# Kernel optimization log

Measured on AMD Instinct MI355X. Metric: run time of the kernel, lower is better.

Reference implementation:

```python
import jax, jax.numpy as jnp
import numpy as np

A = 312          # nb_attributes
LAT = 64         # latent_dim per attribute
HID = 128        # hidden_dim per attribute
OUT = 1          # output_dim per attribute
B = 8192         # batch


def setup_inputs() -> dict:
    key = jax.random.key(0)
    k1, k2, k3, k4, k5 = jax.random.split(key, 5)
    x = jax.random.normal(k1, (B, A * LAT), dtype=jnp.float32)
    # block-diagonal weights: one small matrix per attribute
    W1 = jax.random.normal(k2, (A, LAT, HID), dtype=jnp.float32) * (1.0 / np.sqrt(LAT))
    b1 = jax.random.normal(k3, (A, HID), dtype=jnp.float32) * 0.01
    W2 = jax.random.normal(k4, (A, HID, OUT), dtype=jnp.float32) * (1.0 / np.sqrt(HID))
    b2 = jax.random.normal(k5, (A, OUT), dtype=jnp.float32) * 0.01
    return {"x": x, "W1": W1, "b1": b1, "W2": W2, "b2": b2}


def reference(x, W1, b1, W2, b2):
    # BlockLinear 1: [B, A*LAT] -> view [B, A, LAT] -> per-attribute matmul -> [B, A, HID]
    xb = x.reshape(B, A, LAT)
    h = jnp.einsum('bal,alh->bah', xb, W1) + b1[None]   # [B, A, HID]
    h = jax.nn.relu(h)
    # BlockLinear 2: [B, A, HID] -> [B, A, OUT]
    o = jnp.einsum('bah,aho->bao', h, W2) + b2[None]    # [B, A, OUT]
    o = jax.nn.sigmoid(o)
    return o.reshape(B, A * OUT)
```

## Files before the change

kernel.cpp:

```cpp
#include <hip/hip_runtime.h>
#include <hip/hip_bf16.h>

#define NA   312
#define LAT  64
#define HID  128
#define NB   8192
#define MB   256
#define NBT  (NB / MB)
#define MT   4

typedef __attribute__((ext_vector_type(8))) short bf16x8;
typedef __attribute__((ext_vector_type(4))) float f32x4;

__device__ inline short f2bf(float f) {
    unsigned u = __builtin_bit_cast(unsigned, f);
    u += 0x7FFFu + ((u >> 16) & 1u);
    return (short)(u >> 16);
}

__device__ inline bf16x8 pack8(float4 v0, float4 v1) {
    __hip_bfloat162 c[4] = {
        __float22bfloat162_rn(float2{v0.x, v0.y}),
        __float22bfloat162_rn(float2{v0.z, v0.w}),
        __float22bfloat162_rn(float2{v1.x, v1.y}),
        __float22bfloat162_rn(float2{v1.z, v1.w})};
    bf16x8 f;
    __builtin_memcpy(&f, &c[0], 16);
    return f;
}

__global__ __launch_bounds__(256, 2) void prep_w1(
    const float* __restrict__ W1, short* __restrict__ w1f)
{
    __shared__ float lds[LAT * HID];
    const int a   = blockIdx.x;
    const int tid = threadIdx.x;

    const float4* src = reinterpret_cast<const float4*>(W1 + (size_t)a * (LAT * HID));
    float4* ldsv = reinterpret_cast<float4*>(lds);
    #pragma unroll
    for (int i = 0; i < (LAT * HID / 4) / 256; ++i)
        ldsv[i * 256 + tid] = src[i * 256 + tid];
    __syncthreads();

    bf16x8* dst = reinterpret_cast<bf16x8*>(w1f + (size_t)a * (LAT * HID));
    #pragma unroll
    for (int i = 0; i < 4; ++i) {
        const int e    = i * 256 + tid;
        const int nt   = e >> 7;
        const int kk   = (e >> 6) & 1;
        const int lane = e & 63;
        const int n  = nt * 16 + (lane & 15);
        const int k0 = kk * 32 + (lane >> 4) * 8;
        bf16x8 f;
        #pragma unroll
        for (int j = 0; j < 8; ++j)
            f[j] = f2bf(lds[(k0 + j) * HID + n]);
        dst[e] = f;
    }
}

__global__ __launch_bounds__(256, 2) void attr_decoder_main(
    const float* __restrict__ x,
    const short* __restrict__ w1f,
    const float* __restrict__ b1,
    const float* __restrict__ W2,
    const float* __restrict__ b2,
    float* __restrict__ out)
{
    const unsigned g = blockIdx.x;
    const int a    = g % NA;
    const int bt   = g / NA;
    const int tid  = threadIdx.x;
    const int w    = tid >> 6;
    const int lane = tid & 63;
    const int llo  = lane & 15;
    const int lhi  = lane >> 4;
    const int rowbase = bt * MB + w * 64;

    bf16x8 afrag[MT][2];
    #pragma unroll
    for (int mt = 0; mt < MT; ++mt) {
        const float* xrow = x + (size_t)(rowbase + mt * 16 + llo) * (NA * LAT)
                              + (size_t)a * LAT;
        #pragma unroll
        for (int kk = 0; kk < 2; ++kk) {
            const float4* p = reinterpret_cast<const float4*>(xrow + kk * 32 + lhi * 8);
            afrag[mt][kk] = pack8(p[0], p[1]);
        }
    }

    const bf16x8* wf = reinterpret_cast<const bf16x8*>(w1f + (size_t)a * (LAT * HID));
    const float*  b1a = b1 + a * HID;
    const float*  w2a = W2 + a * HID;
    float p2[MT][4] = {};
    #pragma unroll 4
    for (int nt = 0; nt < 8; ++nt) {
        const bf16x8 bf0 = wf[(nt * 2 + 0) * 64 + lane];
        const bf16x8 bf1 = wf[(nt * 2 + 1) * 64 + lane];
        const int n = nt * 16 + llo;
        const float b1v = b1a[n];
        const float w2v = w2a[n];
        const f32x4 cin = {b1v, b1v, b1v, b1v};
        #pragma unroll
        for (int mt = 0; mt < MT; ++mt) {
            f32x4 acc = cin;
            acc = __builtin_amdgcn_mfma_f32_16x16x32_bf16(afrag[mt][0], bf0, acc, 0, 0, 0);
            acc = __builtin_amdgcn_mfma_f32_16x16x32_bf16(afrag[mt][1], bf1, acc, 0, 0, 0);
            #pragma unroll
            for (int r = 0; r < 4; ++r)
                p2[mt][r] = fmaf(fmaxf(acc[r], 0.f), w2v, p2[mt][r]);
        }
    }

    const float ob = b2[a];
    #pragma unroll
    for (int mt = 0; mt < MT; ++mt) {
        #pragma unroll
        for (int r = 0; r < 4; ++r) {
            float s = p2[mt][r];
            s += __shfl_xor(s, 1);
            s += __shfl_xor(s, 2);
            s += __shfl_xor(s, 4);
            s += __shfl_xor(s, 8);
            s = 1.0f / (1.0f + __expf(-(s + ob)));
            if (llo == 0) {
                const int row = rowbase + mt * 16 + lhi * 4 + r;
                out[(size_t)row * NA + a] = s;
            }
        }
    }
}

extern "C" void kernel_launch(void* const* d_in, const int* in_sizes, int n_in,
                              void* d_out, int out_size, void* d_ws, size_t ws_size,
                              hipStream_t stream) {
    const float* x  = (const float*)d_in[0];
    const float* W1 = (const float*)d_in[1];
    const float* b1 = (const float*)d_in[2];
    const float* W2 = (const float*)d_in[3];
    const float* b2 = (const float*)d_in[4];
    float* out = (float*)d_out;
    short* w1f = (short*)d_ws;

    hipLaunchKernelGGL(prep_w1, dim3(NA), dim3(256), 0, stream, W1, w1f);
    hipLaunchKernelGGL(attr_decoder_main, dim3(NA * NBT), dim3(256), 0, stream,
                       x, w1f, b1, W2, b2, out);
}
```

Baseline: 181.3 us.

## Stage x tiles through LDS with direct global-to-LDS loads, one attribute per wave

Each block now covers 32 rows and a group of 8 attributes. The x tile is loaded contiguously into LDS with global_load_lds and an XOR swizzle, and each of the 8 waves then builds its bf16 A fragments for its own attribute from LDS. This replaces the strided 256-byte-per-row global reads of the old kernel with fully contiguous 2 KB row segments, aiming for better DRAM and cache efficiency on the dominant x stream. In exchange, W1 fragments are re-fetched for every 32-row tile rather than every 256 rows, there is less MFMA work per wave, and the launch now runs many more small blocks.

```diff
diff --git a/kernel.cpp b/kernel.cpp
--- a/kernel.cpp
+++ b/kernel.cpp
@@ -5,9 +5,10 @@
 #define LAT  64
 #define HID  128
 #define NB   8192
-#define MB   256
-#define NBT  (NB / MB)
-#define MT   4
+#define AG   8
+#define NAG  (NA / AG)
+#define RB   32
+#define NBT  (NB / RB)
 
 typedef __attribute__((ext_vector_type(8))) short bf16x8;
 typedef __attribute__((ext_vector_type(4))) float f32x4;
@@ -60,7 +61,7 @@
     }
 }
 
-__global__ __launch_bounds__(256, 2) void attr_decoder_main(
+__global__ __launch_bounds__(512, 4) void attr_decoder_main(
     const float* __restrict__ x,
     const short* __restrict__ w1f,
     const float* __restrict__ b1,
@@ -68,45 +69,67 @@
     const float* __restrict__ b2,
     float* __restrict__ out)
 {
+    __shared__ float xs[RB * AG * LAT];
+
+    const int tid  = threadIdx.x;
     const unsigned g = blockIdx.x;
-    const int a    = g % NA;
-    const int bt   = g / NA;
-    const int tid  = threadIdx.x;
+    const int ag   = g % NAG;
+    const int bt   = g / NAG;
+    const int row0 = bt * RB;
     const int w    = tid >> 6;
     const int lane = tid & 63;
-    const int llo  = lane & 15;
-    const int lhi  = lane >> 4;
-    const int rowbase = bt * MB + w * 64;
 
-    bf16x8 afrag[MT][2];
     #pragma unroll
-    for (int mt = 0; mt < MT; ++mt) {
-        const float* xrow = x + (size_t)(rowbase + mt * 16 + llo) * (NA * LAT)
-                              + (size_t)a * LAT;
+    for (int i = 0; i < 8; ++i) {
+        const int r = w * 4 + (i >> 1);
+        const int p = (i & 1) * 64 + lane;
+        const int c = p ^ (r & 7);
+        const float* src = x + (size_t)(row0 + r) * (NA * LAT)
+                             + ag * (AG * LAT) + c * 4;
+        __builtin_amdgcn_global_load_lds(
+            (const __attribute__((address_space(1))) unsigned*)src,
+            (__attribute__((address_space(3))) unsigned*)&xs[r * (AG * LAT) + (i & 1) * 256],
+            16, 0, 0);
+    }
+    asm volatile("s_waitcnt vmcnt(0)" ::: "memory");
+    __syncthreads();
+
+    const int llo = lane & 15;
+    const int lhi = lane >> 4;
+    const int al  = w;
+    const int a   = ag * AG + al;
+
+    bf16x8 af[2][2];
+    #pragma unroll
+    for (int mt = 0; mt < 2; ++mt) {
+        const int r = mt * 16 + llo;
+        const float* rowp = xs + r * (AG * LAT);
+        const int e = r & 7;
         #pragma unroll
         for (int kk = 0; kk < 2; ++kk) {
-            const float4* p = reinterpret_cast<const float4*>(xrow + kk * 32 + lhi * 8);
-            afrag[mt][kk] = pack8(p[0], p[1]);
+            const int c0 = al * 16 + kk * 8 + lhi * 2;
+            const float4 v0 = *reinterpret_cast<const float4*>(rowp + (size_t)((c0       ^ e) * 4));
+            const float4 v1 = *reinterpret_cast<const float4*>(rowp + (size_t)(((c0 + 1) ^ e) * 4));
+            af[mt][kk] = pack8(v0, v1);
         }
     }
 
-    const bf16x8* wf = reinterpret_cast<const bf16x8*>(w1f + (size_t)a * (LAT * HID));
+    const bf16x8* wf  = reinterpret_cast<const bf16x8*>(w1f + (size_t)a * (LAT * HID));
     const float*  b1a = b1 + a * HID;
     const float*  w2a = W2 + a * HID;
-    float p2[MT][4] = {};
-    #pragma unroll 4
+    float p2[2][4] = {};
+    #pragma unroll
     for (int nt = 0; nt < 8; ++nt) {
         const bf16x8 bf0 = wf[(nt * 2 + 0) * 64 + lane];
         const bf16x8 bf1 = wf[(nt * 2 + 1) * 64 + lane];
         const int n = nt * 16 + llo;
         const float b1v = b1a[n];
         const float w2v = w2a[n];
-        const f32x4 cin = {b1v, b1v, b1v, b1v};
         #pragma unroll
-        for (int mt = 0; mt < MT; ++mt) {
-            f32x4 acc = cin;
-            acc = __builtin_amdgcn_mfma_f32_16x16x32_bf16(afrag[mt][0], bf0, acc, 0, 0, 0);
-            acc = __builtin_amdgcn_mfma_f32_16x16x32_bf16(afrag[mt][1], bf1, acc, 0, 0, 0);
+        for (int mt = 0; mt < 2; ++mt) {
+            f32x4 acc = {b1v, b1v, b1v, b1v};
+            acc = __builtin_amdgcn_mfma_f32_16x16x32_bf16(af[mt][0], bf0, acc, 0, 0, 0);
+            acc = __builtin_amdgcn_mfma_f32_16x16x32_bf16(af[mt][1], bf1, acc, 0, 0, 0);
             #pragma unroll
             for (int r = 0; r < 4; ++r)
                 p2[mt][r] = fmaf(fmaxf(acc[r], 0.f), w2v, p2[mt][r]);
@@ -115,7 +138,7 @@
 
     const float ob = b2[a];
     #pragma unroll
-    for (int mt = 0; mt < MT; ++mt) {
+    for (int mt = 0; mt < 2; ++mt) {
         #pragma unroll
         for (int r = 0; r < 4; ++r) {
             float s = p2[mt][r];
@@ -125,7 +148,7 @@
             s += __shfl_xor(s, 8);
             s = 1.0f / (1.0f + __expf(-(s + ob)));
             if (llo == 0) {
-                const int row = rowbase + mt * 16 + lhi * 4 + r;
+                const int row = row0 + mt * 16 + lhi * 4 + r;
                 out[(size_t)row * NA + a] = s;
             }
         }
@@ -144,6 +167,6 @@
     short* w1f = (short*)d_ws;
 
     hipLaunchKernelGGL(prep_w1, dim3(NA), dim3(256), 0, stream, W1, w1f);
-    hipLaunchKernelGGL(attr_decoder_main, dim3(NA * NBT), dim3(256), 0, stream,
+    hipLaunchKernelGGL(attr_decoder_main, dim3(NAG * NBT), dim3(512), 0, stream,
                        x, w1f, b1, W2, b2, out);
 }
```

Measured after the change: 284.0 us. 1.57x slower.
